# Kernel optimization log

Hardware: AMD Instinct MI355X
Metric: run time of the kernel (lower is better)

## Reference

```python
import jax, jax.numpy as jnp
import numpy as np

B, N, D_IN, D_OUT, H = 8, 1024, 768, 768, 12
D_HEAD = D_OUT // H  # 64; per-head softmax scale is sqrt(D_HEAD)


def setup_inputs() -> dict:
    key = jax.random.key(0)
    kx, kq, kk, kv, kwo, kbo = jax.random.split(key, 6)
    s_in = 1.0 / np.sqrt(D_IN)
    s_out = 1.0 / np.sqrt(D_OUT)
    return {
        "x": jax.random.normal(kx, (B, N, D_IN), dtype=jnp.float32),
        # stacked per-head Linear weights, torch layout [out, in] -> [H, d_head, D_IN]
        "Wq": jax.random.uniform(kq, (H, D_HEAD, D_IN), jnp.float32, -s_in, s_in),
        "Wk": jax.random.uniform(kk, (H, D_HEAD, D_IN), jnp.float32, -s_in, s_in),
        "Wv": jax.random.uniform(kv, (H, D_HEAD, D_IN), jnp.float32, -s_in, s_in),
        "Wo": jax.random.uniform(kwo, (D_OUT, D_OUT), jnp.float32, -s_out, s_out),
        "bo": jax.random.uniform(kbo, (D_OUT,), jnp.float32, -s_out, s_out),
    }


def reference(x, Wq, Wk, Wv, Wo, bo):
    # Per-head projections, batched over heads: [B, H, N, d_head]
    q = jnp.einsum('bnd,hed->bhne', x, Wq)
    k = jnp.einsum('bnd,hed->bhne', x, Wk)
    v = jnp.einsum('bnd,hed->bhne', x, Wv)
    scale = 1.0 / np.sqrt(D_HEAD)
    scores = jnp.einsum('bhie,bhje->bhij', q, k) * scale  # [B, H, N, N]
    att = jax.nn.softmax(scores, axis=-1)
    out = jnp.einsum('bhij,bhje->bhie', att, v)  # [B, H, N, d_head]
    # concat heads along last dim: [B, N, H*d_head]
    out = out.transpose(0, 2, 1, 3).reshape(B, N, D_OUT)
    return out @ Wo.T + bo
```

## Files before the change

kernel.cpp:

```cpp
#include <hip/hip_runtime.h>
#include <hip/hip_bf16.h>


typedef unsigned short u16;
typedef __attribute__((ext_vector_type(8))) short bf8;
typedef __attribute__((ext_vector_type(4))) float f4;
typedef __attribute__((ext_vector_type(4))) unsigned short us4;

#define NB 8
#define NSEQ 1024
#define DMODEL 768
#define NHEAD 12
#define DHEAD 64

#define XELEMS   (NB * NSEQ * DMODEL)
#define WELEMS   (DMODEL * DMODEL)

__device__ __forceinline__ float b2f(u16 u) {
  union { unsigned int i; float f; } c; c.i = ((unsigned int)u) << 16; return c.f;
}
__device__ __forceinline__ u16 f2b(float f) {
  union { float f; unsigned int i; } c; c.f = f;
  unsigned int r = c.i + 0x7fffu + ((c.i >> 16) & 1u);
  return (u16)(r >> 16);
}
__device__ __forceinline__ void gl_lds16(const u16* g, u16* l) {
  __builtin_amdgcn_global_load_lds(
      (const __attribute__((address_space(1))) unsigned int*)g,
      (__attribute__((address_space(3))) unsigned int*)l, 16, 0, 0);
}

struct CvtArgs {
  const float* src[5];
  u16* dst[5];
};
#define G0 (XELEMS / 4)
#define GW (WELEMS / 4)
#define GTOT (G0 + 4 * GW)

__global__ __launch_bounds__(256) void cvt_kernel(CvtArgs a) {
  size_t g = (size_t)blockIdx.x * 256 + threadIdx.x;
  if (g >= GTOT) return;
  int t; size_t off;
  if (g < G0) { t = 0; off = g; }
  else { size_t r = g - G0; t = 1 + (int)(r / GW); off = r % GW; }
  f4 v = *(const f4*)(a.src[t] + off * 4);
  us4 o;
  o[0] = f2b(v[0]); o[1] = f2b(v[1]); o[2] = f2b(v[2]); o[3] = f2b(v[3]);
  *(us4*)(a.dst[t] + off * 4) = o;
}

__global__ __launch_bounds__(256) void qkv_gemm(
    const u16* __restrict__ x, const u16* __restrict__ Wq,
    const u16* __restrict__ Wk, const u16* __restrict__ Wv,
    u16* __restrict__ q, u16* __restrict__ k, u16* __restrict__ vt)
{
  __shared__ __align__(16) u16 lA[128 * 64];
  __shared__ __align__(16) u16 lB[128 * 64];

  const int tid  = threadIdx.x;
  const int lane = tid & 63;
  const int w    = tid >> 6;
  const int wm   = w >> 1, wn = w & 1;
  const int col  = lane & 15;
  const int quad = lane >> 4;
  const int bm = blockIdx.x;
  const int bn = blockIdx.y;

  const int m0 = bm * 128;
  const int proj = bn / 6;
  const u16* Wsel = (proj == 0) ? Wq : (proj == 1 ? Wk : Wv);
  const int nrem0 = (bn % 6) * 128;

  const int krow = lane >> 3;
  const int gsrc = (lane & 7) ^ krow;
  const u16* gA0 = x    + (size_t)(m0    + w * 32 + krow) * DMODEL + gsrc * 8;
  const u16* gB0 = Wsel + (size_t)(nrem0 + w * 32 + krow) * DMODEL + gsrc * 8;

  f4 acc[4][4];
#pragma unroll
  for (int i = 0; i < 4; i++)
#pragma unroll
    for (int j = 0; j < 4; j++) acc[i][j] = (f4)0.0f;

  for (int kk = 0; kk < DMODEL; kk += 64) {
    __syncthreads();
#pragma unroll
    for (int i = 0; i < 4; i++) {
      gl_lds16(gA0 + (size_t)(i * 8) * DMODEL + kk, lA + (w * 32 + i * 8) * 64);
      gl_lds16(gB0 + (size_t)(i * 8) * DMODEL + kk, lB + (w * 32 + i * 8) * 64);
    }
    __syncthreads();

#pragma unroll
    for (int kt = 0; kt < 2; kt++) {
      bf8 af[4], bfr[4];
#pragma unroll
      for (int mt = 0; mt < 4; mt++) {
        const int row = wm * 64 + mt * 16 + col;
        af[mt] = *(const bf8*)&lA[row * 64 + (((kt * 4 + quad) ^ (row & 7)) << 3)];
      }
#pragma unroll
      for (int nt = 0; nt < 4; nt++) {
        const int row = wn * 64 + nt * 16 + col;
        bfr[nt] = *(const bf8*)&lB[row * 64 + (((kt * 4 + quad) ^ (row & 7)) << 3)];
      }
#pragma unroll
      for (int mt = 0; mt < 4; mt++)
#pragma unroll
        for (int nt = 0; nt < 4; nt++)
          acc[mt][nt] = __builtin_amdgcn_mfma_f32_16x16x32_bf16(af[mt], bfr[nt], acc[mt][nt], 0, 0, 0);
    }
  }

  const int mw0 = m0 + wm * 64, nw0 = nrem0 + wn * 64;
  if (proj == 2) {
#pragma unroll
    for (int mt = 0; mt < 4; mt++) {
#pragma unroll
      for (int nt = 0; nt < 4; nt++) {
        const int nc = nw0 + nt * 16 + col;
        const int h = nc >> 6, e = nc & 63;
        const int t0 = mw0 + mt * 16 + quad * 4;
        const int b = t0 >> 10, tok0 = t0 & 1023;
        us4 pk;
#pragma unroll
        for (int r = 0; r < 4; r++) pk[r] = f2b(acc[mt][nt][r]);
        *(us4*)(vt + ((size_t)(b * NHEAD + h) * DHEAD + e) * NSEQ + tok0) = pk;
      }
    }
  } else {
    u16* dst = (proj == 0) ? q : k;
#pragma unroll
    for (int mt = 0; mt < 4; mt++) {
#pragma unroll
      for (int nt = 0; nt < 4; nt++) {
        const int nc = nw0 + nt * 16 + col;
        const int h = nc >> 6, e = nc & 63;
#pragma unroll
        for (int r = 0; r < 4; r++) {
          const int t = mw0 + mt * 16 + quad * 4 + r;
          const int b = t >> 10, tok = t & 1023;
          dst[((size_t)(b * NHEAD + h) * NSEQ + tok) * DHEAD + e] = f2b(acc[mt][nt][r]);
        }
      }
    }
  }
}

__global__ __launch_bounds__(256) void attn_kernel(
    const u16* __restrict__ q, const u16* __restrict__ k,
    const u16* __restrict__ vt, u16* __restrict__ attn)
{
  __shared__ __align__(16) u16 ldsK[128 * 64];
  __shared__ __align__(16) u16 ldsV[64 * 128];
  __shared__ __align__(16) u16 ldsP[4][32 * 128];

  const int tid  = threadIdx.x;
  const int lane = tid & 63;
  const int w    = tid >> 6;
  const int col  = lane & 15;
  const int quad = lane >> 4;
  const int qc = blockIdx.x, h = blockIdx.y, b = blockIdx.z;
  const size_t head = ((size_t)b * NHEAD + h) * NSEQ * DHEAD;
  const int q0 = qc * 128 + w * 32;

  const int krow = lane >> 3;
  const int kgsw = (lane & 7) ^ krow;
  const int vrow = lane >> 4;

  bf8 qf[2][2];
#pragma unroll
  for (int mt = 0; mt < 2; mt++)
#pragma unroll
    for (int kt = 0; kt < 2; kt++) {
      const int row = q0 + mt * 16 + col;
      bf8 t = *(const bf8*)(q + head + (size_t)row * DHEAD + kt * 32 + quad * 8);
#pragma unroll
      for (int j = 0; j < 8; j++) t[j] = (short)f2b(b2f((u16)t[j]) * 0.125f);
      qf[mt][kt] = t;
    }

  float l_[2][4];
  f4 o[2][4];
#pragma unroll
  for (int mt = 0; mt < 2; mt++) {
#pragma unroll
    for (int r = 0; r < 4; r++) l_[mt][r] = 0.0f;
#pragma unroll
    for (int et = 0; et < 4; et++) o[mt][et] = (f4)0.0f;
  }

  for (int t = 0; t < NSEQ / 128; t++) {
    const int kbase = t * 128;

    __syncthreads();
#pragma unroll
    for (int i = 0; i < 4; i++) {
      const int li = w * 4 + i;
      gl_lds16(k + head + (size_t)(kbase + li * 8 + krow) * DHEAD + kgsw * 8,
               &ldsK[li * 512]);
      const int vr = li * 4 + vrow;
      const int vgsw = (lane & 15) ^ (vr & 7);
      gl_lds16(vt + head + (size_t)vr * NSEQ + kbase + vgsw * 8,
               &ldsV[li * 512]);
    }
    __syncthreads();

    f4 s[2][8];
#pragma unroll
    for (int mt = 0; mt < 2; mt++)
#pragma unroll
      for (int nt = 0; nt < 8; nt++) s[mt][nt] = (f4)0.0f;
#pragma unroll
    for (int kt = 0; kt < 2; kt++) {
      bf8 kf[8];
#pragma unroll
      for (int nt = 0; nt < 8; nt++) {
        const int row = nt * 16 + col;
        kf[nt] = *(const bf8*)&ldsK[row * 64 + (((kt * 4 + quad) ^ (col & 7)) << 3)];
      }
#pragma unroll
      for (int mt = 0; mt < 2; mt++)
#pragma unroll
        for (int nt = 0; nt < 8; nt++)
          s[mt][nt] = __builtin_amdgcn_mfma_f32_16x16x32_bf16(qf[mt][kt], kf[nt], s[mt][nt], 0, 0, 0);
    }

#pragma unroll
    for (int mt = 0; mt < 2; mt++)
#pragma unroll
      for (int nt = 0; nt < 8; nt++)
#pragma unroll
        for (int r = 0; r < 4; r++) {
          const float p = __expf(s[mt][nt][r]);
          l_[mt][r] += p;
          const int prow = mt * 16 + quad * 4 + r;
          const int pc   = nt * 16 + col;
          ldsP[w][prow * 128 + ((((pc >> 3) ^ (prow & 7)) << 3) | (pc & 7))] = f2b(p);
        }

#pragma unroll
    for (int kt2 = 0; kt2 < 4; kt2++) {
      bf8 pf[2], vf[4];
#pragma unroll
      for (int mt = 0; mt < 2; mt++)
        pf[mt] = *(const bf8*)&ldsP[w][(mt * 16 + col) * 128 +
                                       (((kt2 * 4 + quad) ^ (col & 7)) << 3)];
#pragma unroll
      for (int et = 0; et < 4; et++) {
        const int row = et * 16 + col;
        vf[et] = *(const bf8*)&ldsV[row * 128 + (((kt2 * 4 + quad) ^ (col & 7)) << 3)];
      }
#pragma unroll
      for (int mt = 0; mt < 2; mt++)
#pragma unroll
        for (int et = 0; et < 4; et++)
          o[mt][et] = __builtin_amdgcn_mfma_f32_16x16x32_bf16(pf[mt], vf[et], o[mt][et], 0, 0, 0);
    }
  }

#pragma unroll
  for (int mt = 0; mt < 2; mt++)
#pragma unroll
    for (int r = 0; r < 4; r++) {
      float sum = l_[mt][r];
      sum += __shfl_xor(sum, 1, 64);
      sum += __shfl_xor(sum, 2, 64);
      sum += __shfl_xor(sum, 4, 64);
      sum += __shfl_xor(sum, 8, 64);
      const float inv = 1.0f / sum;
      const int token = q0 + mt * 16 + quad * 4 + r;
#pragma unroll
      for (int et = 0; et < 4; et++)
        attn[(size_t)(b * NSEQ + token) * DMODEL + h * DHEAD + et * 16 + col] =
            f2b(o[mt][et][r] * inv);
    }
}

__global__ __launch_bounds__(256) void out_gemm(
    const u16* __restrict__ attn, const u16* __restrict__ Wo,
    const float* __restrict__ bo, float* __restrict__ out)
{
  __shared__ __align__(16) u16 lA[128 * 64];
  __shared__ __align__(16) u16 lB[128 * 64];

  const int tid  = threadIdx.x;
  const int lane = tid & 63;
  const int w    = tid >> 6;
  const int wm   = w >> 1, wn = w & 1;
  const int col  = lane & 15;
  const int quad = lane >> 4;
  const int bm = blockIdx.x;
  const int bn = blockIdx.y;

  const int m0 = bm * 128;
  const int n0 = bn * 128;

  const int krow = lane >> 3;
  const int gsrc = (lane & 7) ^ krow;
  const u16* gA0 = attn + (size_t)(m0 + w * 32 + krow) * DMODEL + gsrc * 8;
  const u16* gB0 = Wo   + (size_t)(n0 + w * 32 + krow) * DMODEL + gsrc * 8;

  f4 acc[4][4];
#pragma unroll
  for (int i = 0; i < 4; i++)
#pragma unroll
    for (int j = 0; j < 4; j++) acc[i][j] = (f4)0.0f;

  for (int kk = 0; kk < DMODEL; kk += 64) {
    __syncthreads();
#pragma unroll
    for (int i = 0; i < 4; i++) {
      gl_lds16(gA0 + (size_t)(i * 8) * DMODEL + kk, lA + (w * 32 + i * 8) * 64);
      gl_lds16(gB0 + (size_t)(i * 8) * DMODEL + kk, lB + (w * 32 + i * 8) * 64);
    }
    __syncthreads();

#pragma unroll
    for (int kt = 0; kt < 2; kt++) {
      bf8 af[4], bfr[4];
#pragma unroll
      for (int mt = 0; mt < 4; mt++) {
        const int row = wm * 64 + mt * 16 + col;
        af[mt] = *(const bf8*)&lA[row * 64 + (((kt * 4 + quad) ^ (row & 7)) << 3)];
      }
#pragma unroll
      for (int nt = 0; nt < 4; nt++) {
        const int row = wn * 64 + nt * 16 + col;
        bfr[nt] = *(const bf8*)&lB[row * 64 + (((kt * 4 + quad) ^ (row & 7)) << 3)];
      }
#pragma unroll
      for (int mt = 0; mt < 4; mt++)
#pragma unroll
        for (int nt = 0; nt < 4; nt++)
          acc[mt][nt] = __builtin_amdgcn_mfma_f32_16x16x32_bf16(af[mt], bfr[nt], acc[mt][nt], 0, 0, 0);
    }
  }

  const int mw0 = m0 + wm * 64, nw0 = n0 + wn * 64;
#pragma unroll
  for (int mt = 0; mt < 4; mt++)
#pragma unroll
    for (int nt = 0; nt < 4; nt++) {
      const int n = nw0 + nt * 16 + col;
      const float bias = bo[n];
#pragma unroll
      for (int r = 0; r < 4; r++) {
        const int row = mw0 + mt * 16 + quad * 4 + r;
        out[(size_t)row * DMODEL + n] = acc[mt][nt][r] + bias;
      }
    }
}

extern "C" void kernel_launch(void* const* d_in, const int* in_sizes, int n_in,
                              void* d_out, int out_size, void* d_ws, size_t ws_size,
                              hipStream_t stream) {
  const float* x  = (const float*)d_in[0];
  const float* Wq = (const float*)d_in[1];
  const float* Wk = (const float*)d_in[2];
  const float* Wv = (const float*)d_in[3];
  const float* Wo = (const float*)d_in[4];
  const float* bo = (const float*)d_in[5];
  float* out = (float*)d_out;

  u16* xb   = (u16*)d_ws;
  u16* wqb  = xb  + XELEMS;
  u16* wkb  = wqb + WELEMS;
  u16* wvb  = wkb + WELEMS;
  u16* wob  = wvb + WELEMS;
  u16* q    = wob + WELEMS;
  u16* k    = q   + XELEMS;
  u16* vt   = k   + XELEMS;
  u16* attn = vt  + XELEMS;

  CvtArgs ca;
  ca.src[0] = x;  ca.src[1] = Wq;  ca.src[2] = Wk;  ca.src[3] = Wv;  ca.src[4] = Wo;
  ca.dst[0] = xb; ca.dst[1] = wqb; ca.dst[2] = wkb; ca.dst[3] = wvb; ca.dst[4] = wob;

  cvt_kernel<<<dim3((GTOT + 255) / 256), 256, 0, stream>>>(ca);
  qkv_gemm<<<dim3(64, 18), 256, 0, stream>>>(xb, wqb, wkb, wvb, q, k, vt);
  attn_kernel<<<dim3(8, NHEAD, NB), 256, 0, stream>>>(q, k, vt, attn);
  out_gemm<<<dim3(64, 6), 256, 0, stream>>>(attn, wob, bo, out);
}
```

Before: 227.6 us.

## Shrink attention P staging buffer to padded per-mt tile and flatten grid

The attention kernel now writes the softmax probabilities for one 16-row m-tile at a time into a padded (stride 132) LDS buffer and immediately consumes it in the PV MFMAs. This replaces the full 32x128 XOR-swizzled staging buffer. The change cuts LDS use per block, which may allow more resident blocks, and relies on padding rather than swizzling to avoid bank conflicts. The grid is also flattened to 1D with the batch-head index varying fastest, which changes how blocks are scheduled across K/V data. In exchange, the padded rows need two 8-byte reads per fragment instead of one 16-byte read.

```diff
diff --git a/kernel.cpp b/kernel.cpp
--- a/kernel.cpp
+++ b/kernel.cpp
@@ -4,6 +4,7 @@
 
 typedef unsigned short u16;
 typedef __attribute__((ext_vector_type(8))) short bf8;
+typedef __attribute__((ext_vector_type(4))) short bf4;
 typedef __attribute__((ext_vector_type(4))) float f4;
 typedef __attribute__((ext_vector_type(4))) unsigned short us4;
 
@@ -15,6 +16,8 @@
 
 #define XELEMS   (NB * NSEQ * DMODEL)
 #define WELEMS   (DMODEL * DMODEL)
+
+#define PSTRIDE 132
 
 __device__ __forceinline__ float b2f(u16 u) {
   union { unsigned int i; float f; } c; c.i = ((unsigned int)u) << 16; return c.f;
@@ -154,14 +157,18 @@
 {
   __shared__ __align__(16) u16 ldsK[128 * 64];
   __shared__ __align__(16) u16 ldsV[64 * 128];
-  __shared__ __align__(16) u16 ldsP[4][32 * 128];
+  __shared__ __align__(16) u16 ldsP[4][16][PSTRIDE];
 
   const int tid  = threadIdx.x;
   const int lane = tid & 63;
   const int w    = tid >> 6;
   const int col  = lane & 15;
   const int quad = lane >> 4;
-  const int qc = blockIdx.x, h = blockIdx.y, b = blockIdx.z;
+
+  const int idx = blockIdx.x;
+  const int bh = idx % 96, qc = idx / 96;
+  const int b = bh / 12, h = bh % 12;
+
   const size_t head = ((size_t)b * NHEAD + h) * NSEQ * DHEAD;
   const int q0 = qc * 128 + w * 32;
 
@@ -228,35 +235,33 @@
     }
 
 #pragma unroll
-    for (int mt = 0; mt < 2; mt++)
+    for (int mt = 0; mt < 2; mt++) {
 #pragma unroll
       for (int nt = 0; nt < 8; nt++)
 #pragma unroll
         for (int r = 0; r < 4; r++) {
           const float p = __expf(s[mt][nt][r]);
           l_[mt][r] += p;
-          const int prow = mt * 16 + quad * 4 + r;
-          const int pc   = nt * 16 + col;
-          ldsP[w][prow * 128 + ((((pc >> 3) ^ (prow & 7)) << 3) | (pc & 7))] = f2b(p);
+          ldsP[w][quad * 4 + r][nt * 16 + col] = f2b(p);
         }
-
-#pragma unroll
-    for (int kt2 = 0; kt2 < 4; kt2++) {
-      bf8 pf[2], vf[4];
-#pragma unroll
-      for (int mt = 0; mt < 2; mt++)
-        pf[mt] = *(const bf8*)&ldsP[w][(mt * 16 + col) * 128 +
-                                       (((kt2 * 4 + quad) ^ (col & 7)) << 3)];
-#pragma unroll
-      for (int et = 0; et < 4; et++) {
-        const int row = et * 16 + col;
-        vf[et] = *(const bf8*)&ldsV[row * 128 + (((kt2 * 4 + quad) ^ (col & 7)) << 3)];
-      }
-#pragma unroll
-      for (int mt = 0; mt < 2; mt++)
+#pragma unroll
+      for (int kt2 = 0; kt2 < 4; kt2++) {
+        bf8 pf, vf[4];
+        {
+          const u16* pp = &ldsP[w][col][kt2 * 32 + quad * 8];
+          bf4 lo = *(const bf4*)pp;
+          bf4 hi = *(const bf4*)(pp + 4);
+          pf = bf8{lo[0], lo[1], lo[2], lo[3], hi[0], hi[1], hi[2], hi[3]};
+        }
+#pragma unroll
+        for (int et = 0; et < 4; et++) {
+          const int row = et * 16 + col;
+          vf[et] = *(const bf8*)&ldsV[row * 128 + (((kt2 * 4 + quad) ^ (col & 7)) << 3)];
+        }
 #pragma unroll
         for (int et = 0; et < 4; et++)
-          o[mt][et] = __builtin_amdgcn_mfma_f32_16x16x32_bf16(pf[mt], vf[et], o[mt][et], 0, 0, 0);
+          o[mt][et] = __builtin_amdgcn_mfma_f32_16x16x32_bf16(pf, vf[et], o[mt][et], 0, 0, 0);
+      }
     }
   }
 
@@ -380,6 +385,6 @@
 
   cvt_kernel<<<dim3((GTOT + 255) / 256), 256, 0, stream>>>(ca);
   qkv_gemm<<<dim3(64, 18), 256, 0, stream>>>(xb, wqb, wkb, wvb, q, k, vt);
-  attn_kernel<<<dim3(8, NHEAD, NB), 256, 0, stream>>>(q, k, vt, attn);
+  attn_kernel<<<dim3(768), 256, 0, stream>>>(q, k, vt, attn);
   out_gemm<<<dim3(64, 6), 256, 0, stream>>>(attn, wob, bo, out);
 }
```

After: 208.7 us. -8.3%, faster.
